# Kernel optimization log

Hardware: AMD Instinct MI355X
Metric: run time of the kernel (lower is better)

The kernel has to match this reference:

```python
import math
import jax, jax.numpy as jnp
import numpy as np

N = 4096        # num nodes
IN_DIM = 512
H0 = 64         # hidden_dim[0]
H1 = 64         # hidden_dim[-1]
HEADS = 4
N_CLASSES = 10


def setup_inputs() -> dict:
    key = jax.random.key(0)
    ks = jax.random.split(key, 10)
    feats = jax.random.normal(ks[0], (N, IN_DIM), dtype=jnp.float32)
    counting_attn = jax.random.uniform(ks[1], (N, N), dtype=jnp.float32)
    s1 = 1.0 / math.sqrt(IN_DIM)
    s2 = 1.0 / math.sqrt(H0 * HEADS)
    # layer-1 heads, stacked: [H, out, in] (torch Linear weight layout)
    Wq1 = jax.random.normal(ks[2], (HEADS, H0, IN_DIM), dtype=jnp.float32) * s1
    Wk1 = jax.random.normal(ks[3], (HEADS, H0, IN_DIM), dtype=jnp.float32) * s1
    Wv1 = jax.random.normal(ks[4], (HEADS, H0, IN_DIM), dtype=jnp.float32) * s1
    # layer-2 single head: [out, in]
    Wq2 = jax.random.normal(ks[5], (H1, H0 * HEADS), dtype=jnp.float32) * s2
    Wk2 = jax.random.normal(ks[6], (H1, H0 * HEADS), dtype=jnp.float32) * s2
    Wv2 = jax.random.normal(ks[7], (H1, H0 * HEADS), dtype=jnp.float32) * s2
    Wc = jax.random.normal(ks[8], (N_CLASSES, H1), dtype=jnp.float32) * (1.0 / math.sqrt(H1))
    bc = jax.random.normal(ks[9], (N_CLASSES,), dtype=jnp.float32) * 0.01
    return {"feats": feats, "counting_attn": counting_attn,
            "Wq1": Wq1, "Wk1": Wk1, "Wv1": Wv1,
            "Wq2": Wq2, "Wk2": Wk2, "Wv2": Wv2,
            "Wc": Wc, "bc": bc}


def _gkat_heads(feat, Wq, Wk, Wv, counting):
    # feat: [N, in], Wq/Wk/Wv: [H, d, in], counting: [N, N] -> [N, H*d]
    Q = jnp.einsum('ni,hdi->hnd', feat, Wq)
    K = jnp.einsum('ni,hdi->hnd', feat, Wk)
    V = jnp.einsum('ni,hdi->hnd', feat, Wv)
    d = Q.shape[-1]
    logits = jnp.einsum('hnd,hmd->hnm', Q, K) / jnp.sqrt(jnp.asarray(d, Q.dtype))
    e = jnp.exp(logits - jnp.max(logits, axis=-1, keepdims=True))
    a = jnp.einsum('hnm,mk->hnk', e, counting)          # exp(logits) @ counting_attn
    a = a / (jnp.sum(a, axis=-1, keepdims=True) + 1e-9)  # row-normalize
    ret = jnp.einsum('hnm,hmd->hnd', a, V)
    ret = jax.nn.elu(ret)
    H, n, dd = ret.shape
    return jnp.transpose(ret, (1, 0, 2)).reshape(n, H * dd)  # concat heads along dim=1


def reference(feats, counting_attn, Wq1, Wk1, Wv1, Wq2, Wk2, Wv2, Wc, bc):
    # normalize over feature dim (torch.std is unbiased -> ddof=1)
    mean_ = jnp.mean(feats, axis=1, keepdims=True)
    std_ = jnp.std(feats, axis=1, keepdims=True, ddof=1)
    h = (feats - mean_) / (std_ + 1e-9)
    h = _gkat_heads(h, Wq1, Wk1, Wv1, counting_attn)                 # [N, H*H0]
    h = _gkat_heads(h, Wq2[None], Wk2[None], Wv2[None], counting_attn)  # [N, H1]
    return h @ Wc.T + bc
```

## Files before the change

### kernel.cpp

```cpp
#include <hip/hip_runtime.h>
#include <hip/hip_bf16.h>
#include <math.h>

#define NN4   4096

typedef __attribute__((ext_vector_type(8))) short short8;
typedef __attribute__((ext_vector_type(8))) unsigned short ushort8;
typedef __attribute__((ext_vector_type(4))) unsigned short ushort4v;
typedef __attribute__((ext_vector_type(4))) float f32x4;

__device__ __forceinline__ unsigned short f2b(float f) {
  union { __hip_bfloat16 h; unsigned short u; } v;
  v.h = __float2bfloat16(f);
  return v.u;
}
__device__ __forceinline__ float b2f(unsigned short s) {
  return __uint_as_float(((unsigned int)s) << 16);
}
__device__ __forceinline__ ushort8 cvt8(f32x4 a, f32x4 b) {
  return (ushort8){f2b(a[0]), f2b(a[1]), f2b(a[2]), f2b(a[3]),
                   f2b(b[0]), f2b(b[1]), f2b(b[2]), f2b(b[3])};
}

#define GLOAD16(gp, lp) __builtin_amdgcn_global_load_lds( \
    (const __attribute__((address_space(1))) void*)(gp),  \
    (__attribute__((address_space(3))) void*)(lp), 16, 0, 0)

__global__ __launch_bounds__(256) void k_norm(const float* __restrict__ x,
                                              unsigned short* __restrict__ y) {
  int row  = blockIdx.x * 4 + (threadIdx.x >> 6);
  int lane = threadIdx.x & 63;
  const float4* src = (const float4*)(x + (size_t)row * 512);
  float4 a = src[lane];
  float4 b = src[lane + 64];
  float s = a.x + a.y + a.z + a.w + b.x + b.y + b.z + b.w;
#pragma unroll
  for (int off = 32; off; off >>= 1) s += __shfl_xor(s, off);
  float mean = s * (1.0f / 512.0f);
  float ssq = 0.f, d;
  d = a.x - mean; ssq += d * d;  d = a.y - mean; ssq += d * d;
  d = a.z - mean; ssq += d * d;  d = a.w - mean; ssq += d * d;
  d = b.x - mean; ssq += d * d;  d = b.y - mean; ssq += d * d;
  d = b.z - mean; ssq += d * d;  d = b.w - mean; ssq += d * d;
#pragma unroll
  for (int off = 32; off; off >>= 1) ssq += __shfl_xor(ssq, off);
  float inv = 1.0f / (sqrtf(ssq * (1.0f / 511.0f)) + 1e-9f);
  unsigned short* dst = y + (size_t)row * 512;
  ushort4v va = (ushort4v){f2b((a.x - mean) * inv), f2b((a.y - mean) * inv),
                           f2b((a.z - mean) * inv), f2b((a.w - mean) * inv)};
  ushort4v vb = (ushort4v){f2b((b.x - mean) * inv), f2b((b.y - mean) * inv),
                           f2b((b.z - mean) * inv), f2b((b.w - mean) * inv)};
  *(ushort4v*)(dst + lane * 4)       = va;
  *(ushort4v*)(dst + 256 + lane * 4) = vb;
}

__global__ __launch_bounds__(256) void k_projqkv(
    const unsigned short* __restrict__ Ap, int K,
    const float* __restrict__ Wq, const float* __restrict__ Wk,
    const float* __restrict__ Wv, int N, int nT,
    unsigned short* __restrict__ Qo, unsigned short* __restrict__ Ko,
    unsigned short* __restrict__ VT, int padrows, float qscale) {
  __shared__ unsigned short As[128 * 40];
  __shared__ unsigned short Bs[128 * 40];
  const int tid = threadIdx.x;
  const int sel = blockIdx.y / nT;
  const int n0 = (blockIdx.y % nT) * 128;
  const int m0 = blockIdx.x * 128;
  const float* Bp = sel == 0 ? Wq : (sel == 1 ? Wk : Wv);
  const float bscale = sel == 0 ? qscale : 1.0f;
  const int lane = tid & 63, wid = tid >> 6;
  const int hi = lane >> 4, lo = lane & 15;
  const int wr = (wid >> 1) << 6, wc = (wid & 1) << 6;
  const int srow = tid >> 1, sk = (tid & 1) << 4;
  f32x4 acc[4][4];
#pragma unroll
  for (int i = 0; i < 4; ++i)
#pragma unroll
    for (int j = 0; j < 4; ++j) acc[i][j] = (f32x4){0.f, 0.f, 0.f, 0.f};

  for (int k0 = 0; k0 < K; k0 += 32) {
    ushort8 va0, va1, vb0, vb1;
    {
      const unsigned short* s = Ap + (size_t)(m0 + srow) * K + k0 + sk;
      va0 = *(const ushort8*)(s);
      va1 = *(const ushort8*)(s + 8);
    }
    {
      int gr = n0 + srow;
      if (gr < N) {
        const float* s = Bp + (size_t)gr * K + k0 + sk;
        f32x4 f0 = *(const f32x4*)(s) * bscale;
        f32x4 f1 = *(const f32x4*)(s + 4) * bscale;
        f32x4 f2 = *(const f32x4*)(s + 8) * bscale;
        f32x4 f3 = *(const f32x4*)(s + 12) * bscale;
        vb0 = cvt8(f0, f1); vb1 = cvt8(f2, f3);
      } else { vb0 = (ushort8)0; vb1 = (ushort8)0; }
    }
    __syncthreads();
    *(ushort8*)&As[srow * 40 + sk]     = va0;
    *(ushort8*)&As[srow * 40 + sk + 8] = va1;
    *(ushort8*)&Bs[srow * 40 + sk]     = vb0;
    *(ushort8*)&Bs[srow * 40 + sk + 8] = vb1;
    __syncthreads();
    short8 af[4], bf[4];
#pragma unroll
    for (int i = 0; i < 4; ++i)
      af[i] = *(const short8*)&As[(wr + (i << 4) + lo) * 40 + hi * 8];
#pragma unroll
    for (int j = 0; j < 4; ++j)
      bf[j] = *(const short8*)&Bs[(wc + (j << 4) + lo) * 40 + hi * 8];
#pragma unroll
    for (int i = 0; i < 4; ++i)
#pragma unroll
      for (int j = 0; j < 4; ++j)
        acc[i][j] = __builtin_amdgcn_mfma_f32_16x16x32_bf16(af[i], bf[j], acc[i][j], 0, 0, 0);
  }

  if (sel < 2) {
    unsigned short* Cp = sel == 0 ? Qo : Ko;
#pragma unroll
    for (int i = 0; i < 4; ++i)
#pragma unroll
      for (int j = 0; j < 4; ++j)
#pragma unroll
        for (int reg = 0; reg < 4; ++reg) {
          int r = m0 + wr + (i << 4) + (hi << 2) + reg;
          int c = n0 + wc + (j << 4) + lo;
          if (c < N) Cp[(size_t)r * N + c] = f2b(acc[i][j][reg]);
        }
  } else {
#pragma unroll
    for (int i = 0; i < 4; ++i)
#pragma unroll
      for (int j = 0; j < 4; ++j) {
        int c = n0 + wc + (j << 4) + lo;
        if (c < N) {
          int hh = c >> 6, dd = c & 63;
          int rb = m0 + wr + (i << 4) + (hi << 2);
          ushort4v pk = (ushort4v){f2b(acc[i][j][0]), f2b(acc[i][j][1]),
                                   f2b(acc[i][j][2]), f2b(acc[i][j][3])};
          *(ushort4v*)&VT[(size_t)(hh * 68 + dd) * NN4 + rb] = pk;
        }
      }
    int hstart = n0 >> 6;
    int hcnt = (N - n0) >> 6; if (hcnt > 2) hcnt = 2;
    int tot = hcnt * padrows * 128;
    for (int e = tid; e < tot; e += 256) {
      int hh = hstart + e / (padrows * 128);
      int rem = e % (padrows * 128);
      int j = rem >> 7, col = m0 + (rem & 127);
      VT[(size_t)(hh * 68 + 64 + j) * NN4 + col] = (j == 0) ? 0x3F80 : 0;
    }
  }
}

template<int NF>
__global__ __launch_bounds__(256, 2) void k_cvxg(
    const float* __restrict__ cnt,
    const unsigned short* __restrict__ Bt,
    unsigned short* __restrict__ Pb) {
  constexpr int LDB = NF * 16;
  __shared__ unsigned short As[2][128 * 40];
  __shared__ unsigned short Bs[2][LDB * 32];
  const int tid = threadIdx.x, lane = tid & 63, wid = tid >> 6;
  const int hi = lane >> 4, lo = lane & 15;
  const int m0 = blockIdx.x * 128;
  const int kbeg = blockIdx.y << 8, kend = kbeg + 256;
  const int arow = tid >> 1, ak = (tid & 1) << 4;
  const int boff = (lo * 64 + hi * 16) ^ (((lo >> 1) & 3) << 4);

  f32x4 acc[2][NF];
#pragma unroll
  for (int i = 0; i < 2; ++i)
#pragma unroll
    for (int j = 0; j < NF; ++j) acc[i][j] = (f32x4){0.f, 0.f, 0.f, 0.f};

  f32x4 ar0, ar1, ar2, ar3;
  {
    const float* s = cnt + (size_t)(m0 + arow) * 4096 + kbeg + ak;
    ar0 = *(const f32x4*)(s);     ar1 = *(const f32x4*)(s + 4);
    ar2 = *(const f32x4*)(s + 8); ar3 = *(const f32x4*)(s + 12);
  }
  for (int c = wid; c < NF; c += 4) {
    int P = c * 1024 + lane * 16;
    int L = P ^ ((P >> 3) & 0x30);
    GLOAD16(Bt + (size_t)(L >> 6) * 4096 + kbeg + ((L & 63) >> 1),
            (char*)&Bs[0][0] + c * 1024);
  }
  *(ushort8*)&As[0][arow * 40 + ak]     = cvt8(ar0, ar1);
  *(ushort8*)&As[0][arow * 40 + ak + 8] = cvt8(ar2, ar3);
  asm volatile("s_waitcnt vmcnt(0)" ::: "memory");
  __syncthreads();

  for (int k0 = kbeg; k0 < kend; k0 += 32) {
    const int cur = ((k0 - kbeg) >> 5) & 1, nxt = cur ^ 1;
    const bool more = (k0 + 32 < kend);
    if (more) {
      const float* s = cnt + (size_t)(m0 + arow) * 4096 + (k0 + 32) + ak;
      ar0 = *(const f32x4*)(s);     ar1 = *(const f32x4*)(s + 4);
      ar2 = *(const f32x4*)(s + 8); ar3 = *(const f32x4*)(s + 12);
      for (int c = wid; c < NF; c += 4) {
        int P = c * 1024 + lane * 16;
        int L = P ^ ((P >> 3) & 0x30);
        GLOAD16(Bt + (size_t)(L >> 6) * 4096 + (k0 + 32) + ((L & 63) >> 1),
                (char*)&Bs[nxt][0] + c * 1024);
      }
    }
    short8 af0 = *(const short8*)&As[cur][(32 * wid + lo) * 40 + hi * 8];
    short8 af1 = *(const short8*)&As[cur][(32 * wid + 16 + lo) * 40 + hi * 8];
    __builtin_amdgcn_s_setprio(1);
#pragma unroll
    for (int j = 0; j < NF; ++j) {
      short8 bf = *(const short8*)((const char*)&Bs[cur][0] + j * 1024 + boff);
      acc[0][j] = __builtin_amdgcn_mfma_f32_16x16x32_bf16(af0, bf, acc[0][j], 0, 0, 0);
      acc[1][j] = __builtin_amdgcn_mfma_f32_16x16x32_bf16(af1, bf, acc[1][j], 0, 0, 0);
    }
    __builtin_amdgcn_s_setprio(0);
    if (more) {
      *(ushort8*)&As[nxt][arow * 40 + ak]     = cvt8(ar0, ar1);
      *(ushort8*)&As[nxt][arow * 40 + ak + 8] = cvt8(ar2, ar3);
    }
    asm volatile("s_waitcnt vmcnt(0)" ::: "memory");
    __syncthreads();
  }
  unsigned short* P = Pb + (size_t)blockIdx.y * 4096 * LDB;
#pragma unroll
  for (int i = 0; i < 2; ++i)
#pragma unroll
    for (int j = 0; j < NF; ++j)
#pragma unroll
      for (int reg = 0; reg < 4; ++reg) {
        int r = m0 + 32 * wid + 16 * i + 4 * hi + reg;
        P[(size_t)r * LDB + 16 * j + lo] = f2b(acc[i][j][reg]);
      }
}

__global__ __launch_bounds__(256) void k_tredB(const unsigned short* __restrict__ in, int ld,
                                               int nsl, unsigned short* __restrict__ out,
                                               int orow) {
  __shared__ float t[64][65];
  const int n0 = blockIdx.x << 6, d0 = blockIdx.y << 6;
  const int o  = threadIdx.x & 7;
  const int rr = threadIdx.x >> 3;
  const size_t pstride = (size_t)4096 * ld;
  const bool valid = (o * 8) < (ld - d0);
#pragma unroll
  for (int pass = 0; pass < 2; ++pass) {
    const int r = rr + (pass << 5);
    float a[8] = {0.f, 0.f, 0.f, 0.f, 0.f, 0.f, 0.f, 0.f};
    if (valid) {
      const unsigned short* p = in + (size_t)(n0 + r) * ld + d0 + o * 8;
      for (int z = 0; z < nsl; ++z) {
        ushort8 v = *(const ushort8*)(p + (size_t)z * pstride);
#pragma unroll
        for (int k = 0; k < 8; ++k) a[k] += b2f(v[k]);
      }
    }
#pragma unroll
    for (int k = 0; k < 8; ++k) t[o * 8 + k][r] = a[k];
  }
  __syncthreads();
  const int c = threadIdx.x & 63, r4 = threadIdx.x >> 6;
#pragma unroll
  for (int i = 0; i < 16; ++i) {
    int dr = r4 + (i << 2);
    if (d0 + dr < orow)
      out[(size_t)(d0 + dr) * 4096 + n0 + c] = f2b(t[dr][c]);
  }
}

__global__ __launch_bounds__(256, 2) void k_attn(
    const unsigned short* __restrict__ Qg, const unsigned short* __restrict__ Kg,
    int ldqk, const unsigned short* __restrict__ CVg,
    unsigned short* __restrict__ Pb) {
  __shared__ unsigned short Ks[128 * 72];
  __shared__ unsigned short Cs[80 * 136];
  __shared__ unsigned short Es[128 * 136];
  const int tid = threadIdx.x, lane = tid & 63, wid = tid >> 6;
  const int hi = lane >> 4, lo = lane & 15;
  const int qb = blockIdx.x, h = blockIdx.y, sl = blockIdx.z;
  const int n0 = qb * 128;
  const int MS = 4096 / gridDim.z;
  const int m0beg = sl * MS;
  const int wr = (wid >> 1) << 6, wc = (wid & 1) << 6;

  short8 qf[4][2];
  const unsigned short* Qh = Qg + (size_t)h * 64;
#pragma unroll
  for (int j = 0; j < 4; ++j)
#pragma unroll
    for (int t = 0; t < 2; ++t)
      qf[j][t] = *(const short8*)(Qh + (size_t)(n0 + wc + 16 * j + lo) * ldqk + t * 32 + hi * 8);

  const unsigned short* CVh = CVg + (size_t)h * 68 * NN4;
  const unsigned short* Kh  = Kg + (size_t)h * 64;

  const int krow = tid >> 1, khalf = (tid & 1) << 5;
  int crdR[5], crdW[5], ccol[5];
#pragma unroll
  for (int k = 0; k < 5; ++k) {
    int c = tid + k * 256;
    int row = c >> 4;
    crdW[k] = row;
    crdR[k] = row < 68 ? row : 67;
    ccol[k] = (c & 15) << 3;
  }
  ushort8 krg[4], crg[5];

  auto LOADK = [&](int m0) {
    const unsigned short* src = Kh + (size_t)(m0 + krow) * ldqk + khalf;
    krg[0] = *(const ushort8*)(src);
    krg[1] = *(const ushort8*)(src + 8);
    krg[2] = *(const ushort8*)(src + 16);
    krg[3] = *(const ushort8*)(src + 24);
  };
  auto LOADC = [&](int m0) {
#pragma unroll
    for (int k = 0; k < 5; ++k)
      crg[k] = *(const ushort8*)(CVh + (size_t)crdR[k] * NN4 + m0 + ccol[k]);
  };
  auto WRITEK = [&]() {
    unsigned short* dp = &Ks[krow * 72 + khalf];
    *(ushort8*)(dp) = krg[0];      *(ushort8*)(dp + 8) = krg[1];
    *(ushort8*)(dp + 16) = krg[2]; *(ushort8*)(dp + 24) = krg[3];
  };
  auto WRITEC = [&]() {
#pragma unroll
    for (int k = 0; k < 5; ++k)
      *(ushort8*)&Cs[crdW[k] * 136 + ccol[k]] = crg[k];
  };

  f32x4 accn[2][5];
#pragma unroll
  for (int i = 0; i < 2; ++i)
#pragma unroll
    for (int j = 0; j < 5; ++j) accn[i][j] = (f32x4){0.f, 0.f, 0.f, 0.f};

  LOADK(m0beg); LOADC(m0beg);
  WRITEK(); WRITEC();
  __syncthreads();

  for (int mt = 0; mt < MS; mt += 128) {
    const int m0 = m0beg + mt;
    const bool more = (mt + 128) < MS;
    if (more) { LOADK(m0 + 128); LOADC(m0 + 128); }
    short8 kf[4][2];
#pragma unroll
    for (int i = 0; i < 4; ++i)
#pragma unroll
      for (int t = 0; t < 2; ++t)
        kf[i][t] = *(const short8*)&Ks[(wr + 16 * i + lo) * 72 + t * 32 + hi * 8];
    f32x4 s[4][4];
#pragma unroll
    for (int i = 0; i < 4; ++i)
#pragma unroll
      for (int j = 0; j < 4; ++j) s[i][j] = (f32x4){0.f, 0.f, 0.f, 0.f};
    __builtin_amdgcn_s_setprio(1);
#pragma unroll
    for (int t = 0; t < 2; ++t)
#pragma unroll
      for (int i = 0; i < 4; ++i)
#pragma unroll
        for (int j = 0; j < 4; ++j)
          s[i][j] = __builtin_amdgcn_mfma_f32_16x16x32_bf16(kf[i][t], qf[j][t], s[i][j], 0, 0, 0);
    __builtin_amdgcn_s_setprio(0);
#pragma unroll
    for (int i = 0; i < 4; ++i)
#pragma unroll
      for (int j = 0; j < 4; ++j) {
        unsigned int u0 = (unsigned int)f2b(__expf(s[i][j][0])) |
                          ((unsigned int)f2b(__expf(s[i][j][1])) << 16);
        unsigned int u1 = (unsigned int)f2b(__expf(s[i][j][2])) |
                          ((unsigned int)f2b(__expf(s[i][j][3])) << 16);
        unsigned long long pk = (unsigned long long)u0 | ((unsigned long long)u1 << 32);
        int row = wc + 16 * j + lo;
        int byte = row * 272 + (wr + 16 * i + 4 * hi) * 2;
        *(unsigned long long*)((char*)Es + (byte ^ ((row & 7) << 5))) = pk;
      }
    __syncthreads();
    if (more) WRITEK();
    __builtin_amdgcn_s_setprio(1);
#pragma unroll
    for (int t2 = 0; t2 < 4; ++t2) {
      int r0 = 32 * wid + lo, r1 = r0 + 16;
      int cb = (t2 * 32 + hi * 8) * 2;
      short8 ea0 = *(const short8*)((const char*)Es + ((r0 * 272 + cb) ^ ((r0 & 7) << 5)));
      short8 ea1 = *(const short8*)((const char*)Es + ((r1 * 272 + cb) ^ ((r1 & 7) << 5)));
      short8 cbv[5];
#pragma unroll
      for (int j2 = 0; j2 < 5; ++j2)
        cbv[j2] = *(const short8*)&Cs[(16 * j2 + lo) * 136 + t2 * 32 + hi * 8];
#pragma unroll
      for (int j2 = 0; j2 < 5; ++j2) {
        accn[0][j2] = __builtin_amdgcn_mfma_f32_16x16x32_bf16(ea0, cbv[j2], accn[0][j2], 0, 0, 0);
        accn[1][j2] = __builtin_amdgcn_mfma_f32_16x16x32_bf16(ea1, cbv[j2], accn[1][j2], 0, 0, 0);
      }
    }
    __builtin_amdgcn_s_setprio(0);
    __syncthreads();
    if (more) { WRITEC(); __syncthreads(); }
  }
  unsigned short* P = Pb + (((size_t)h * gridDim.x + qb) * gridDim.z + sl) * (128 * 80);
#pragma unroll
  for (int i2 = 0; i2 < 2; ++i2)
#pragma unroll
    for (int j2 = 0; j2 < 5; ++j2)
#pragma unroll
      for (int reg = 0; reg < 4; ++reg) {
        int r = 32 * wid + 16 * i2 + 4 * hi + reg;
        int c = 16 * j2 + lo;
        P[(size_t)r * 80 + c] = f2b(accn[i2][j2][reg]);
      }
}

__global__ void k_fin2(const unsigned short* __restrict__ parts, int nsl,
                       unsigned short* __restrict__ hb, int ldh) {
  int idx = blockIdx.x * 256 + threadIdx.x;
  int d = idx & 63, r = (idx >> 6) & 4095, h = idx >> 18;
  size_t b0 = ((size_t)(h * 32 + (r >> 7)) * nsl) * 10240 + (size_t)(r & 127) * 80;
  float nm = 0.f, dn = 0.f;
  for (int sl = 0; sl < nsl; ++sl) {
    const unsigned short* p = parts + b0 + (size_t)sl * 10240;
    nm += b2f(p[d]); dn += b2f(p[64]);
  }
  float x = nm / (dn + 1e-9f);
  x = x > 0.f ? x : expm1f(x);
  hb[(size_t)r * ldh + h * 64 + d] = f2b(x);
}

__global__ __launch_bounds__(256) void k_fincls(const unsigned short* __restrict__ parts,
                                                int nsl, const float* __restrict__ Wc,
                                                const float* __restrict__ bc,
                                                float* __restrict__ out) {
  int r = blockIdx.x * 4 + (threadIdx.x >> 6);
  int d = threadIdx.x & 63;
  size_t b0 = ((size_t)(r >> 7) * nsl) * 10240 + (size_t)(r & 127) * 80;
  float nm = 0.f, dn = 0.f;
  for (int sl = 0; sl < nsl; ++sl) {
    const unsigned short* p = parts + b0 + (size_t)sl * 10240;
    nm += b2f(p[d]); dn += b2f(p[64]);
  }
  float x = nm / (dn + 1e-9f);
  x = x > 0.f ? x : expm1f(x);
#pragma unroll
  for (int cl = 0; cl < 10; ++cl) {
    float v = x * Wc[cl * 64 + d];
#pragma unroll
    for (int off = 32; off; off >>= 1) v += __shfl_xor(v, off);
    if (d == 0) out[(size_t)r * 10 + cl] = v + bc[cl];
  }
}

extern "C" void kernel_launch(void* const* d_in, const int* in_sizes, int n_in,
                              void* d_out, int out_size, void* d_ws, size_t ws_size,
                              hipStream_t stream) {
  (void)in_sizes; (void)n_in; (void)out_size; (void)ws_size;
  const float* feats    = (const float*)d_in[0];
  const float* counting = (const float*)d_in[1];
  const float* Wq1 = (const float*)d_in[2];
  const float* Wk1 = (const float*)d_in[3];
  const float* Wv1 = (const float*)d_in[4];
  const float* Wq2 = (const float*)d_in[5];
  const float* Wk2 = (const float*)d_in[6];
  const float* Wv2 = (const float*)d_in[7];
  const float* Wc  = (const float*)d_in[8];
  const float* bc  = (const float*)d_in[9];
  float* out = (float*)d_out;

  char* w = (char*)d_ws;
  size_t off = 0;
  auto alloc = [&](size_t bytes) { void* p = w + off; off += (bytes + 255) & ~(size_t)255; return p; };
  unsigned short* hnb    = (unsigned short*)alloc((size_t)4096 * 512 * 2);
  unsigned short* Q1b    = (unsigned short*)alloc((size_t)4096 * 256 * 2);
  unsigned short* K1b    = (unsigned short*)alloc((size_t)4096 * 256 * 2);
  unsigned short* V1xT   = (unsigned short*)alloc((size_t)272 * 4096 * 2);
  unsigned short* CVX1Tb = (unsigned short*)alloc((size_t)272 * 4096 * 2);
  unsigned short* h1b    = (unsigned short*)alloc((size_t)4096 * 256 * 2);
  unsigned short* Q2b    = (unsigned short*)alloc((size_t)4096 * 64 * 2);
  unsigned short* K2b    = (unsigned short*)alloc((size_t)4096 * 64 * 2);
  unsigned short* V2xT   = (unsigned short*)alloc((size_t)80 * 4096 * 2);
  unsigned short* CVX2Tb = (unsigned short*)alloc((size_t)68 * 4096 * 2);
  unsigned short* big    = (unsigned short*)alloc((size_t)36 * 1024 * 1024);

  k_norm<<<1024, 256, 0, stream>>>(feats, hnb);

  k_projqkv<<<dim3(32, 6), 256, 0, stream>>>(hnb, 512, Wq1, Wk1, Wv1, 256, 2,
                                             Q1b, K1b, V1xT, 4, 0.125f);
  k_cvxg<17><<<dim3(32, 16), 256, 0, stream>>>(counting, V1xT, big);
  k_tredB<<<dim3(64, 5), 256, 0, stream>>>(big, 272, 16, CVX1Tb, 272);
  k_attn<<<dim3(32, 4, 4), 256, 0, stream>>>(Q1b, K1b, 256, CVX1Tb, big);
  k_fin2<<<4096, 256, 0, stream>>>(big, 4, h1b, 256);

  k_projqkv<<<dim3(32, 3), 256, 0, stream>>>(h1b, 256, Wq2, Wk2, Wv2, 64, 1,
                                             Q2b, K2b, V2xT, 16, 0.125f);
  k_cvxg<5><<<dim3(32, 16), 256, 0, stream>>>(counting, V2xT, big);
  k_tredB<<<dim3(64, 2), 256, 0, stream>>>(big, 80, 16, CVX2Tb, 68);
  k_attn<<<dim3(32, 1, 16), 256, 0, stream>>>(Q2b, K2b, 64, CVX2Tb, big);
  k_fincls<<<1024, 256, 0, stream>>>(big, 16, Wc, bc, out);
}
```

Before: 165.1 us.

## Split attention blocks into eight waves and use exp2 with folded log2e scale

The attention kernel now runs 512 threads (8 waves) per block instead of 256. Each wave computes a 64x32 slice of the score tile and a 16-row slice of the output, so per-wave register use (score and accumulator arrays) is halved. That is meant to raise latency hiding and occupancy. The Q projection scale now folds in log2(e), so the exponent can use the native exp2 instruction instead of __expf. The trade-offs are more waves contending for the same LDS tiles and less reuse of K fragments per wave, and the hardware exp2 may be slightly less precise.

```diff
diff --git a/kernel.cpp b/kernel.cpp
--- a/kernel.cpp
+++ b/kernel.cpp
@@ -3,6 +3,7 @@
 #include <math.h>
 
 #define NN4   4096
+#define QSCALE 0.180336880111120420f
 
 typedef __attribute__((ext_vector_type(8))) short short8;
 typedef __attribute__((ext_vector_type(8))) unsigned short ushort8;
@@ -269,7 +270,7 @@
   }
 }
 
-__global__ __launch_bounds__(256, 2) void k_attn(
+__global__ __launch_bounds__(512, 4) void k_attn(
     const unsigned short* __restrict__ Qg, const unsigned short* __restrict__ Kg,
     int ldqk, const unsigned short* __restrict__ CVg,
     unsigned short* __restrict__ Pb) {
@@ -282,59 +283,56 @@
   const int n0 = qb * 128;
   const int MS = 4096 / gridDim.z;
   const int m0beg = sl * MS;
-  const int wr = (wid >> 1) << 6, wc = (wid & 1) << 6;
-
-  short8 qf[4][2];
+  const int aw = wid >> 2, bw = wid & 3;
+
+  short8 qf[2][2];
   const unsigned short* Qh = Qg + (size_t)h * 64;
 #pragma unroll
-  for (int j = 0; j < 4; ++j)
+  for (int j = 0; j < 2; ++j)
 #pragma unroll
     for (int t = 0; t < 2; ++t)
-      qf[j][t] = *(const short8*)(Qh + (size_t)(n0 + wc + 16 * j + lo) * ldqk + t * 32 + hi * 8);
+      qf[j][t] = *(const short8*)(Qh + (size_t)(n0 + bw * 32 + 16 * j + lo) * ldqk + t * 32 + hi * 8);
 
   const unsigned short* CVh = CVg + (size_t)h * 68 * NN4;
   const unsigned short* Kh  = Kg + (size_t)h * 64;
 
-  const int krow = tid >> 1, khalf = (tid & 1) << 5;
-  int crdR[5], crdW[5], ccol[5];
-#pragma unroll
-  for (int k = 0; k < 5; ++k) {
-    int c = tid + k * 256;
-    int row = c >> 4;
+  const int krow = tid >> 2, kq = (tid & 3) << 4;
+  int crdR[3], crdW[3], ccol[3];
+  bool cok[3];
+#pragma unroll
+  for (int k = 0; k < 3; ++k) {
+    int c = tid + k * 512;
+    cok[k] = c < 1280;
+    int row = cok[k] ? (c >> 4) : 0;
     crdW[k] = row;
     crdR[k] = row < 68 ? row : 67;
     ccol[k] = (c & 15) << 3;
   }
-  ushort8 krg[4], crg[5];
+  ushort8 krg[2], crg[3];
 
   auto LOADK = [&](int m0) {
-    const unsigned short* src = Kh + (size_t)(m0 + krow) * ldqk + khalf;
+    const unsigned short* src = Kh + (size_t)(m0 + krow) * ldqk + kq;
     krg[0] = *(const ushort8*)(src);
     krg[1] = *(const ushort8*)(src + 8);
-    krg[2] = *(const ushort8*)(src + 16);
-    krg[3] = *(const ushort8*)(src + 24);
   };
   auto LOADC = [&](int m0) {
 #pragma unroll
-    for (int k = 0; k < 5; ++k)
-      crg[k] = *(const ushort8*)(CVh + (size_t)crdR[k] * NN4 + m0 + ccol[k]);
+    for (int k = 0; k < 3; ++k)
+      if (cok[k]) crg[k] = *(const ushort8*)(CVh + (size_t)crdR[k] * NN4 + m0 + ccol[k]);
   };
   auto WRITEK = [&]() {
-    unsigned short* dp = &Ks[krow * 72 + khalf];
-    *(ushort8*)(dp) = krg[0];      *(ushort8*)(dp + 8) = krg[1];
-    *(ushort8*)(dp + 16) = krg[2]; *(ushort8*)(dp + 24) = krg[3];
+    unsigned short* dp = &Ks[krow * 72 + kq];
+    *(ushort8*)(dp) = krg[0]; *(ushort8*)(dp + 8) = krg[1];
   };
   auto WRITEC = [&]() {
 #pragma unroll
-    for (int k = 0; k < 5; ++k)
-      *(ushort8*)&Cs[crdW[k] * 136 + ccol[k]] = crg[k];
+    for (int k = 0; k < 3; ++k)
+      if (cok[k]) *(ushort8*)&Cs[crdW[k] * 136 + ccol[k]] = crg[k];
   };
 
-  f32x4 accn[2][5];
-#pragma unroll
-  for (int i = 0; i < 2; ++i)
-#pragma unroll
-    for (int j = 0; j < 5; ++j) accn[i][j] = (f32x4){0.f, 0.f, 0.f, 0.f};
+  f32x4 accn[5];
+#pragma unroll
+  for (int j = 0; j < 5; ++j) accn[j] = (f32x4){0.f, 0.f, 0.f, 0.f};
 
   LOADK(m0beg); LOADC(m0beg);
   WRITEK(); WRITEC();
@@ -349,32 +347,32 @@
     for (int i = 0; i < 4; ++i)
 #pragma unroll
       for (int t = 0; t < 2; ++t)
-        kf[i][t] = *(const short8*)&Ks[(wr + 16 * i + lo) * 72 + t * 32 + hi * 8];
-    f32x4 s[4][4];
-#pragma unroll
-    for (int i = 0; i < 4; ++i)
-#pragma unroll
-      for (int j = 0; j < 4; ++j) s[i][j] = (f32x4){0.f, 0.f, 0.f, 0.f};
+        kf[i][t] = *(const short8*)&Ks[(aw * 64 + 16 * i + lo) * 72 + t * 32 + hi * 8];
+    f32x4 s[4][2];
+#pragma unroll
+    for (int i = 0; i < 4; ++i)
+#pragma unroll
+      for (int j = 0; j < 2; ++j) s[i][j] = (f32x4){0.f, 0.f, 0.f, 0.f};
     __builtin_amdgcn_s_setprio(1);
 #pragma unroll
     for (int t = 0; t < 2; ++t)
 #pragma unroll
       for (int i = 0; i < 4; ++i)
 #pragma unroll
-        for (int j = 0; j < 4; ++j)
+        for (int j = 0; j < 2; ++j)
           s[i][j] = __builtin_amdgcn_mfma_f32_16x16x32_bf16(kf[i][t], qf[j][t], s[i][j], 0, 0, 0);
     __builtin_amdgcn_s_setprio(0);
 #pragma unroll
     for (int i = 0; i < 4; ++i)
 #pragma unroll
-      for (int j = 0; j < 4; ++j) {
-        unsigned int u0 = (unsigned int)f2b(__expf(s[i][j][0])) |
-                          ((unsigned int)f2b(__expf(s[i][j][1])) << 16);
-        unsigned int u1 = (unsigned int)f2b(__expf(s[i][j][2])) |
-                          ((unsigned int)f2b(__expf(s[i][j][3])) << 16);
+      for (int j = 0; j < 2; ++j) {
+        unsigned int u0 = (unsigned int)f2b(__builtin_amdgcn_exp2f(s[i][j][0])) |
+                          ((unsigned int)f2b(__builtin_amdgcn_exp2f(s[i][j][1])) << 16);
+        unsigned int u1 = (unsigned int)f2b(__builtin_amdgcn_exp2f(s[i][j][2])) |
+                          ((unsigned int)f2b(__builtin_amdgcn_exp2f(s[i][j][3])) << 16);
         unsigned long long pk = (unsigned long long)u0 | ((unsigned long long)u1 << 32);
-        int row = wc + 16 * j + lo;
-        int byte = row * 272 + (wr + 16 * i + 4 * hi) * 2;
+        int row = bw * 32 + 16 * j + lo;
+        int byte = row * 272 + (aw * 64 + 16 * i + 4 * hi) * 2;
         *(unsigned long long*)((char*)Es + (byte ^ ((row & 7) << 5))) = pk;
       }
     __syncthreads();
@@ -382,19 +380,16 @@
     __builtin_amdgcn_s_setprio(1);
 #pragma unroll
     for (int t2 = 0; t2 < 4; ++t2) {
-      int r0 = 32 * wid + lo, r1 = r0 + 16;
+      int r0 = 16 * wid + lo;
       int cb = (t2 * 32 + hi * 8) * 2;
-      short8 ea0 = *(const short8*)((const char*)Es + ((r0 * 272 + cb) ^ ((r0 & 7) << 5)));
-      short8 ea1 = *(const short8*)((const char*)Es + ((r1 * 272 + cb) ^ ((r1 & 7) << 5)));
+      short8 ea = *(const short8*)((const char*)Es + ((r0 * 272 + cb) ^ ((r0 & 7) << 5)));
       short8 cbv[5];
 #pragma unroll
       for (int j2 = 0; j2 < 5; ++j2)
         cbv[j2] = *(const short8*)&Cs[(16 * j2 + lo) * 136 + t2 * 32 + hi * 8];
 #pragma unroll
-      for (int j2 = 0; j2 < 5; ++j2) {
-        accn[0][j2] = __builtin_amdgcn_mfma_f32_16x16x32_bf16(ea0, cbv[j2], accn[0][j2], 0, 0, 0);
-        accn[1][j2] = __builtin_amdgcn_mfma_f32_16x16x32_bf16(ea1, cbv[j2], accn[1][j2], 0, 0, 0);
-      }
+      for (int j2 = 0; j2 < 5; ++j2)
+        accn[j2] = __builtin_amdgcn_mfma_f32_16x16x32_bf16(ea, cbv[j2], accn[j2], 0, 0, 0);
     }
     __builtin_amdgcn_s_setprio(0);
     __syncthreads();
@@ -402,15 +397,13 @@
   }
   unsigned short* P = Pb + (((size_t)h * gridDim.x + qb) * gridDim.z + sl) * (128 * 80);
 #pragma unroll
-  for (int i2 = 0; i2 < 2; ++i2)
-#pragma unroll
-    for (int j2 = 0; j2 < 5; ++j2)
-#pragma unroll
-      for (int reg = 0; reg < 4; ++reg) {
-        int r = 32 * wid + 16 * i2 + 4 * hi + reg;
-        int c = 16 * j2 + lo;
-        P[(size_t)r * 80 + c] = f2b(accn[i2][j2][reg]);
-      }
+  for (int j2 = 0; j2 < 5; ++j2)
+#pragma unroll
+    for (int reg = 0; reg < 4; ++reg) {
+      int r = 16 * wid + 4 * hi + reg;
+      int c = 16 * j2 + lo;
+      P[(size_t)r * 80 + c] = f2b(accn[j2][reg]);
+    }
 }
 
 __global__ void k_fin2(const unsigned short* __restrict__ parts, int nsl,
@@ -485,16 +478,16 @@
   k_norm<<<1024, 256, 0, stream>>>(feats, hnb);
 
   k_projqkv<<<dim3(32, 6), 256, 0, stream>>>(hnb, 512, Wq1, Wk1, Wv1, 256, 2,
-                                             Q1b, K1b, V1xT, 4, 0.125f);
+                                             Q1b, K1b, V1xT, 4, QSCALE);
   k_cvxg<17><<<dim3(32, 16), 256, 0, stream>>>(counting, V1xT, big);
   k_tredB<<<dim3(64, 5), 256, 0, stream>>>(big, 272, 16, CVX1Tb, 272);
-  k_attn<<<dim3(32, 4, 4), 256, 0, stream>>>(Q1b, K1b, 256, CVX1Tb, big);
+  k_attn<<<dim3(32, 4, 4), 512, 0, stream>>>(Q1b, K1b, 256, CVX1Tb, big);
   k_fin2<<<4096, 256, 0, stream>>>(big, 4, h1b, 256);
 
   k_projqkv<<<dim3(32, 3), 256, 0, stream>>>(h1b, 256, Wq2, Wk2, Wv2, 64, 1,
-                                             Q2b, K2b, V2xT, 16, 0.125f);
+                                             Q2b, K2b, V2xT, 16, QSCALE);
   k_cvxg<5><<<dim3(32, 16), 256, 0, stream>>>(counting, V2xT, big);
   k_tredB<<<dim3(64, 2), 256, 0, stream>>>(big, 80, 16, CVX2Tb, 68);
-  k_attn<<<dim3(32, 1, 16), 256, 0, stream>>>(Q2b, K2b, 64, CVX2Tb, big);
+  k_attn<<<dim3(32, 1, 16), 512, 0, stream>>>(Q2b, K2b, 64, CVX2Tb, big);
   k_fincls<<<1024, 256, 0, stream>>>(big, 16, Wc, bc, out);
 }
```

New measurement: 173.5 us. +5.1%, slower.

## Halve cvxg row tile for more blocks and fold log2e into Q scale for exp2

Applied to the files above, without the earlier changes.

The counting-times-V GEMM kernel now uses 64-row tiles instead of 128, so each wave computes one 16-row MFMA strip. The grid doubles to 64x16 blocks and launch bounds allow 3 blocks per CU, raising occupancy and parallelism on this memory-bound pass over the 4096x4096 fp32 counting matrix. Separately, the Q scale now includes log2(e), so the attention kernel can call the hardware exp2 instruction directly instead of __expf. The cost is that each B tile loaded into LDS is reused by half as many rows, which increases B reloads and per-block overhead.

```diff
diff --git a/kernel.cpp b/kernel.cpp
--- a/kernel.cpp
+++ b/kernel.cpp
@@ -3,6 +3,7 @@
 #include <math.h>
 
 #define NN4   4096
+#define QSCALE 0.180336880111120420f
 
 typedef __attribute__((ext_vector_type(8))) short short8;
 typedef __attribute__((ext_vector_type(8))) unsigned short ushort8;
@@ -155,31 +156,28 @@
 }
 
 template<int NF>
-__global__ __launch_bounds__(256, 2) void k_cvxg(
+__global__ __launch_bounds__(256, 3) void k_cvxg(
     const float* __restrict__ cnt,
     const unsigned short* __restrict__ Bt,
     unsigned short* __restrict__ Pb) {
   constexpr int LDB = NF * 16;
-  __shared__ unsigned short As[2][128 * 40];
+  __shared__ unsigned short As[2][64 * 40];
   __shared__ unsigned short Bs[2][LDB * 32];
   const int tid = threadIdx.x, lane = tid & 63, wid = tid >> 6;
   const int hi = lane >> 4, lo = lane & 15;
-  const int m0 = blockIdx.x * 128;
+  const int m0 = blockIdx.x * 64;
   const int kbeg = blockIdx.y << 8, kend = kbeg + 256;
-  const int arow = tid >> 1, ak = (tid & 1) << 4;
+  const int arow = tid >> 2, ak = (tid & 3) << 3;
   const int boff = (lo * 64 + hi * 16) ^ (((lo >> 1) & 3) << 4);
 
-  f32x4 acc[2][NF];
-#pragma unroll
-  for (int i = 0; i < 2; ++i)
-#pragma unroll
-    for (int j = 0; j < NF; ++j) acc[i][j] = (f32x4){0.f, 0.f, 0.f, 0.f};
-
-  f32x4 ar0, ar1, ar2, ar3;
+  f32x4 acc[NF];
+#pragma unroll
+  for (int j = 0; j < NF; ++j) acc[j] = (f32x4){0.f, 0.f, 0.f, 0.f};
+
+  f32x4 ar0, ar1;
   {
     const float* s = cnt + (size_t)(m0 + arow) * 4096 + kbeg + ak;
-    ar0 = *(const f32x4*)(s);     ar1 = *(const f32x4*)(s + 4);
-    ar2 = *(const f32x4*)(s + 8); ar3 = *(const f32x4*)(s + 12);
+    ar0 = *(const f32x4*)(s); ar1 = *(const f32x4*)(s + 4);
   }
   for (int c = wid; c < NF; c += 4) {
     int P = c * 1024 + lane * 16;
@@ -187,8 +185,7 @@
     GLOAD16(Bt + (size_t)(L >> 6) * 4096 + kbeg + ((L & 63) >> 1),
             (char*)&Bs[0][0] + c * 1024);
   }
-  *(ushort8*)&As[0][arow * 40 + ak]     = cvt8(ar0, ar1);
-  *(ushort8*)&As[0][arow * 40 + ak + 8] = cvt8(ar2, ar3);
+  *(ushort8*)&As[0][arow * 40 + ak] = cvt8(ar0, ar1);
   asm volatile("s_waitcnt vmcnt(0)" ::: "memory");
   __syncthreads();
 
@@ -197,8 +194,7 @@
     const bool more = (k0 + 32 < kend);
     if (more) {
       const float* s = cnt + (size_t)(m0 + arow) * 4096 + (k0 + 32) + ak;
-      ar0 = *(const f32x4*)(s);     ar1 = *(const f32x4*)(s + 4);
-      ar2 = *(const f32x4*)(s + 8); ar3 = *(const f32x4*)(s + 12);
+      ar0 = *(const f32x4*)(s); ar1 = *(const f32x4*)(s + 4);
       for (int c = wid; c < NF; c += 4) {
         int P = c * 1024 + lane * 16;
         int L = P ^ ((P >> 3) & 0x30);
@@ -206,33 +202,26 @@
                 (char*)&Bs[nxt][0] + c * 1024);
       }
     }
-    short8 af0 = *(const short8*)&As[cur][(32 * wid + lo) * 40 + hi * 8];
-    short8 af1 = *(const short8*)&As[cur][(32 * wid + 16 + lo) * 40 + hi * 8];
+    short8 af0 = *(const short8*)&As[cur][(16 * wid + lo) * 40 + hi * 8];
     __builtin_amdgcn_s_setprio(1);
 #pragma unroll
     for (int j = 0; j < NF; ++j) {
       short8 bf = *(const short8*)((const char*)&Bs[cur][0] + j * 1024 + boff);
-      acc[0][j] = __builtin_amdgcn_mfma_f32_16x16x32_bf16(af0, bf, acc[0][j], 0, 0, 0);
-      acc[1][j] = __builtin_amdgcn_mfma_f32_16x16x32_bf16(af1, bf, acc[1][j], 0, 0, 0);
+      acc[j] = __builtin_amdgcn_mfma_f32_16x16x32_bf16(af0, bf, acc[j], 0, 0, 0);
     }
     __builtin_amdgcn_s_setprio(0);
-    if (more) {
-      *(ushort8*)&As[nxt][arow * 40 + ak]     = cvt8(ar0, ar1);
-      *(ushort8*)&As[nxt][arow * 40 + ak + 8] = cvt8(ar2, ar3);
-    }
+    if (more) *(ushort8*)&As[nxt][arow * 40 + ak] = cvt8(ar0, ar1);
     asm volatile("s_waitcnt vmcnt(0)" ::: "memory");
     __syncthreads();
   }
   unsigned short* P = Pb + (size_t)blockIdx.y * 4096 * LDB;
 #pragma unroll
-  for (int i = 0; i < 2; ++i)
-#pragma unroll
-    for (int j = 0; j < NF; ++j)
-#pragma unroll
-      for (int reg = 0; reg < 4; ++reg) {
-        int r = m0 + 32 * wid + 16 * i + 4 * hi + reg;
-        P[(size_t)r * LDB + 16 * j + lo] = f2b(acc[i][j][reg]);
-      }
+  for (int j = 0; j < NF; ++j)
+#pragma unroll
+    for (int reg = 0; reg < 4; ++reg) {
+      int r = m0 + 16 * wid + 4 * hi + reg;
+      P[(size_t)r * LDB + 16 * j + lo] = f2b(acc[j][reg]);
+    }
 }
 
 __global__ __launch_bounds__(256) void k_tredB(const unsigned short* __restrict__ in, int ld,
@@ -368,10 +357,10 @@
     for (int i = 0; i < 4; ++i)
 #pragma unroll
       for (int j = 0; j < 4; ++j) {
-        unsigned int u0 = (unsigned int)f2b(__expf(s[i][j][0])) |
-                          ((unsigned int)f2b(__expf(s[i][j][1])) << 16);
-        unsigned int u1 = (unsigned int)f2b(__expf(s[i][j][2])) |
-                          ((unsigned int)f2b(__expf(s[i][j][3])) << 16);
+        unsigned int u0 = (unsigned int)f2b(__builtin_amdgcn_exp2f(s[i][j][0])) |
+                          ((unsigned int)f2b(__builtin_amdgcn_exp2f(s[i][j][1])) << 16);
+        unsigned int u1 = (unsigned int)f2b(__builtin_amdgcn_exp2f(s[i][j][2])) |
+                          ((unsigned int)f2b(__builtin_amdgcn_exp2f(s[i][j][3])) << 16);
         unsigned long long pk = (unsigned long long)u0 | ((unsigned long long)u1 << 32);
         int row = wc + 16 * j + lo;
         int byte = row * 272 + (wr + 16 * i + 4 * hi) * 2;
@@ -485,15 +474,15 @@
   k_norm<<<1024, 256, 0, stream>>>(feats, hnb);
 
   k_projqkv<<<dim3(32, 6), 256, 0, stream>>>(hnb, 512, Wq1, Wk1, Wv1, 256, 2,
-                                             Q1b, K1b, V1xT, 4, 0.125f);
-  k_cvxg<17><<<dim3(32, 16), 256, 0, stream>>>(counting, V1xT, big);
+                                             Q1b, K1b, V1xT, 4, QSCALE);
+  k_cvxg<17><<<dim3(64, 16), 256, 0, stream>>>(counting, V1xT, big);
   k_tredB<<<dim3(64, 5), 256, 0, stream>>>(big, 272, 16, CVX1Tb, 272);
   k_attn<<<dim3(32, 4, 4), 256, 0, stream>>>(Q1b, K1b, 256, CVX1Tb, big);
   k_fin2<<<4096, 256, 0, stream>>>(big, 4, h1b, 256);
 
   k_projqkv<<<dim3(32, 3), 256, 0, stream>>>(h1b, 256, Wq2, Wk2, Wv2, 64, 1,
-                                             Q2b, K2b, V2xT, 16, 0.125f);
-  k_cvxg<5><<<dim3(32, 16), 256, 0, stream>>>(counting, V2xT, big);
+                                             Q2b, K2b, V2xT, 16, QSCALE);
+  k_cvxg<5><<<dim3(64, 16), 256, 0, stream>>>(counting, V2xT, big);
   k_tredB<<<dim3(64, 2), 256, 0, stream>>>(big, 80, 16, CVX2Tb, 68);
   k_attn<<<dim3(32, 1, 16), 256, 0, stream>>>(Q2b, K2b, 64, CVX2Tb, big);
   k_fincls<<<1024, 256, 0, stream>>>(big, 16, Wc, bc, out);
```

Result: no change. 167.6 us (+1.5%).
